# Kernel tuning notes

Hardware: AMD Instinct MI355X
Metric: run time of the kernel (lower is better)

## Reference

```python
import jax, jax.numpy as jnp
import numpy as np

D_MODEL = 2048
N_HEADS = 16
D_K = D_MODEL // N_HEADS
MAX_SEQ_LEN = 2048


def _rotary_tables(dim, max_seq_len):
    angular_freq = (1.0 / 10000.0) ** jnp.linspace(0.0, 1.0, dim // 2, dtype=jnp.float32)
    t = jnp.arange(max_seq_len, dtype=jnp.float32)
    theta = jnp.einsum('i,j->ij', t, angular_freq)  # [S, dk/2]
    return jnp.cos(theta), jnp.sin(theta)


def _apply_rotary(x, cos, sin):
    # x: [B, H, S, dk]; cos/sin: [S, dk/2]
    seq_len = x.shape[-2]
    c = cos[:seq_len][None, None]
    s = sin[:seq_len][None, None]
    x1, x2 = jnp.split(x, 2, axis=-1)
    y1 = x1 * c - x2 * s
    y2 = x1 * s + x2 * c
    return jnp.concatenate([y1, y2], axis=-1).astype(x.dtype)


def setup_inputs() -> dict:
    key = jax.random.key(0)
    k_x, k_qkv, k_o = jax.random.split(key, 3)
    B, S = 2, 2048
    x = jax.random.normal(k_x, (B, S, D_MODEL), dtype=jnp.float32)
    scale = 1.0 / np.sqrt(D_MODEL)
    w_qkv = jax.random.normal(k_qkv, (3 * D_MODEL, D_MODEL), dtype=jnp.float32) * scale
    w_o = jax.random.normal(k_o, (D_MODEL, D_MODEL), dtype=jnp.float32) * scale
    return {"x": x, "w_qkv": w_qkv, "w_o": w_o}


def reference(x, w_qkv, w_o):
    B, S, _ = x.shape
    cos, sin = _rotary_tables(D_K, MAX_SEQ_LEN)
    qkv = jnp.einsum('bsd,ed->bse', x, w_qkv)  # [B, S, 3*d_model]
    qkv = qkv.reshape(B, S, 3, N_HEADS, D_K).transpose(2, 0, 3, 1, 4)  # [3,B,H,S,dk]
    Q, K, V = qkv[0], qkv[1], qkv[2]
    Q = _apply_rotary(Q, cos, sin)
    K = _apply_rotary(K, cos, sin)
    scale = 1.0 / np.sqrt(D_K)
    scores = jnp.einsum('bhqd,bhkd->bhqk', Q, K) * scale
    causal = jnp.tril(jnp.ones((S, S), dtype=bool))
    scores = jnp.where(causal[None, None], scores, jnp.finfo(scores.dtype).min)
    attn = jax.nn.softmax(scores, axis=-1)
    out = jnp.einsum('bhqk,bhkd->bhqd', attn, V)  # [B,H,S,dk]
    out = out.transpose(0, 2, 1, 3).reshape(B, S, D_MODEL)
    return jnp.einsum('bsd,ed->bse', out, w_o)
```

## Files before the change

kernel.cpp:

```cpp
#include <hip/hip_runtime.h>
#include <hip/hip_bf16.h>


typedef __bf16 bf16;
typedef __bf16 bf16x4 __attribute__((ext_vector_type(4)));
typedef __bf16 bf16x8 __attribute__((ext_vector_type(8)));
typedef float f32x4 __attribute__((ext_vector_type(4)));
typedef float f32x16 __attribute__((ext_vector_type(16)));
typedef int i32x4 __attribute__((ext_vector_type(4)));

#define DEV __device__ __forceinline__

DEV void gll16(const void* g, void* lds_base_wave_uniform) {
  __builtin_amdgcn_global_load_lds((const __attribute__((address_space(1))) void*)g,
                                   (__attribute__((address_space(3))) void*)lds_base_wave_uniform,
                                   16, 0, 0);
}

DEV f32x4 mfma16(bf16x8 a, bf16x8 b, f32x4 c) {
  return __builtin_amdgcn_mfma_f32_16x16x32_bf16(a, b, c, 0, 0, 0);
}
DEV f32x16 mfma32(bf16x8 a, bf16x8 b, f32x16 c) {
  return __builtin_amdgcn_mfma_f32_32x32x16_bf16(a, b, c, 0, 0, 0);
}

DEV int cvtpk(float lo, float hi) {
  int r;
  asm("v_cvt_pk_bf16_f32 %0, %1, %2" : "=v"(r) : "v"(lo), "v"(hi));
  return r;
}

__global__ __launch_bounds__(256) void prep_all(const float* __restrict__ x,
                                                const float* __restrict__ wqkv,
                                                const float* __restrict__ wo,
                                                bf16* __restrict__ xb,
                                                bf16* __restrict__ wqkvb,
                                                bf16* __restrict__ wob,
                                                float* __restrict__ ctab,
                                                float* __restrict__ stab) {
  const int b = blockIdx.x;
  if (b < 12288) {
    const float* in;
    bf16* out;
    int bb = b;
    if (b < 4096) {
      in = x; out = xb;
    } else if (b < 10240) {
      in = wqkv; out = wqkvb; bb -= 4096;
    } else {
      in = wo; out = wob; bb -= 10240;
    }
    const int i = (bb * 256 + threadIdx.x) << 3;
    float4 a = *(const float4*)(in + i);
    float4 c = *(const float4*)(in + i + 4);
    bf16x8 o;
    o[0] = (bf16)a.x; o[1] = (bf16)a.y; o[2] = (bf16)a.z; o[3] = (bf16)a.w;
    o[4] = (bf16)c.x; o[5] = (bf16)c.y; o[6] = (bf16)c.z; o[7] = (bf16)c.w;
    *(bf16x8*)(out + i) = o;
  } else {
    const int id = (b - 12288) * 256 + threadIdx.x;
    const int s = id >> 6, j = id & 63;
    float freq = powf(10000.0f, -(float)j / 63.0f);
    float th = (float)s * freq;
    ctab[id] = cosf(th);
    stab[id] = sinf(th);
  }
}

__global__ __launch_bounds__(512, 2) void gemm384(const bf16* __restrict__ A,
                                                  const bf16* __restrict__ Bt,
                                                  bf16* __restrict__ q_out,
                                                  bf16* __restrict__ k_out,
                                                  bf16* __restrict__ v_out,
                                                  const float* __restrict__ ctab,
                                                  const float* __restrict__ stab) {
  constexpr int K = 2048, NKT = 64;
  constexpr int BUFB = 40960;
  __shared__ char lds[3 * BUFB];
  const int id = blockIdx.x;
  const int swz = (id & 7) * 32 + (id >> 3);
  const int bx = swz & 15, by = swz >> 4;
  const int m0 = by << 8;
  const int n0 = bx * 384;
  const int tid = threadIdx.x, w = tid >> 6, l = tid & 63;
  const int wm = w >> 2, wn = w & 3;
  const int lsl = (l & 7) ^ ((l >> 3) & 7);
  const int srow = ((l >> 3) << 1) + (lsl >> 2);
  const int scol = (lsl & 3) << 3;

  auto STAGE = [&](int t, char* base) {
    const int k0 = t << 5;
#pragma unroll
    for (int c = 0; c < 2; ++c) {
      const int row = (c << 7) + (w << 4) + srow;
      gll16(A + (size_t)(m0 + row) * K + k0 + scol, base + (c << 13) + (w << 10));
    }
#pragma unroll
    for (int c = 0; c < 3; ++c) {
      const int row = (c << 7) + (w << 4) + srow;
      gll16(Bt + (size_t)(n0 + row) * K + k0 + scol, base + 16384 + (c << 13) + (w << 10));
    }
  };

  f32x4 acc[8][6] = {};

  STAGE(0, (char*)lds);
  STAGE(1, (char*)lds + BUFB);
  asm volatile("s_waitcnt vmcnt(5)" ::: "memory");
  __builtin_amdgcn_s_barrier();

#pragma unroll 1
  for (int t = 0, bi = 0, bj = 2; t < NKT; ++t) {
    char* rbase = (char*)lds + bi * BUFB;
    bf16x8 bfr[6];
#pragma unroll
    for (int j = 0; j < 6; ++j) {
      const int row = ((j >> 1) << 7) + ((j & 1) << 6) + (wn << 4) + (l & 15);
      const int sr = row >> 1;
      bfr[j] = *(const bf16x8*)(rbase + 16384 + sr * 128 +
                                (((((row & 1) << 2) | (l >> 4)) ^ (sr & 7)) << 4));
    }
    bf16x8 af[4];
#pragma unroll
    for (int i = 0; i < 4; ++i) {
      const int row = (wm << 7) + (i << 4) + (l & 15);
      const int sr = row >> 1;
      af[i] = *(const bf16x8*)(rbase + sr * 128 +
                               (((((row & 1) << 2) | (l >> 4)) ^ (sr & 7)) << 4));
    }
    if (t + 2 < NKT) STAGE(t + 2, (char*)lds + bj * BUFB);
    asm volatile("s_waitcnt lgkmcnt(0)" ::: "memory");
    __builtin_amdgcn_sched_barrier(0);
    __builtin_amdgcn_s_setprio(1);
#pragma unroll
    for (int i = 0; i < 4; ++i)
#pragma unroll
      for (int j = 0; j < 6; ++j)
        acc[i][j] = mfma16(af[i], bfr[j], acc[i][j]);
    __builtin_amdgcn_s_setprio(0);
#pragma unroll
    for (int i = 0; i < 4; ++i) {
      const int row = (wm << 7) + 64 + (i << 4) + (l & 15);
      const int sr = row >> 1;
      af[i] = *(const bf16x8*)(rbase + sr * 128 +
                               (((((row & 1) << 2) | (l >> 4)) ^ (sr & 7)) << 4));
    }
    asm volatile("s_waitcnt lgkmcnt(0)" ::: "memory");
    __builtin_amdgcn_sched_barrier(0);
    __builtin_amdgcn_s_setprio(1);
#pragma unroll
    for (int i = 0; i < 4; ++i)
#pragma unroll
      for (int j = 0; j < 6; ++j)
        acc[4 + i][j] = mfma16(af[i], bfr[j], acc[4 + i][j]);
    __builtin_amdgcn_s_setprio(0);
    if (t + 2 < NKT) {
      asm volatile("s_waitcnt vmcnt(5)" ::: "memory");
    } else if (t + 2 == NKT) {
      asm volatile("s_waitcnt vmcnt(0)" ::: "memory");
    }
    __builtin_amdgcn_sched_barrier(0);
    __builtin_amdgcn_s_barrier();
    bi = (bi == 2) ? 0 : bi + 1;
    bj = (bj == 2) ? 0 : bj + 1;
  }

  const int d2 = (wn << 4) + (l & 15);
#pragma unroll
  for (int i = 0; i < 8; ++i) {
    const int mbase = m0 + (wm << 7) + (i << 4) + ((l >> 4) << 2);
    const int b_ = mbase >> 11, sbase = mbase & 2047;
    float cc[4], ss[4];
    if (((n0 + 256) >> 11) == 1 || (n0 >> 11) == 1) {
#pragma unroll
      for (int r = 0; r < 4; ++r) {
        cc[r] = ctab[((sbase + r) << 6) + d2];
        ss[r] = stab[((sbase + r) << 6) + d2];
      }
    }
#pragma unroll
    for (int p = 0; p < 3; ++p) {
      const int nb = n0 + (p << 7);
      const int which = nb >> 11;
      const int h = (nb >> 7) & 15;
      if (which == 0) {
        const size_t base = (((size_t)((b_ << 4) | h)) * 2048 + sbase) * 128;
#pragma unroll
        for (int r = 0; r < 4; ++r) {
          q_out[base + ((size_t)r << 7) + d2]      = (bf16)acc[i][2 * p][r];
          q_out[base + ((size_t)r << 7) + d2 + 64] = (bf16)acc[i][2 * p + 1][r];
        }
      } else if (which == 1) {
        const size_t base = (((size_t)((b_ << 4) | h)) * 2048 + sbase) * 128;
#pragma unroll
        for (int r = 0; r < 4; ++r) {
          const float x1 = acc[i][2 * p][r], x2 = acc[i][2 * p + 1][r];
          k_out[base + ((size_t)r << 7) + d2]      = (bf16)(x1 * cc[r] - x2 * ss[r]);
          k_out[base + ((size_t)r << 7) + d2 + 64] = (bf16)(x1 * ss[r] + x2 * cc[r]);
        }
      } else {
        bf16x4 v1, v2;
#pragma unroll
        for (int r = 0; r < 4; ++r) {
          v1[r] = (bf16)acc[i][2 * p][r];
          v2[r] = (bf16)acc[i][2 * p + 1][r];
        }
        const size_t hb = ((size_t)((b_ << 4) | h) << 18);
        *(bf16x4*)(v_out + hb + ((size_t)d2 << 11) + sbase) = v1;
        *(bf16x4*)(v_out + hb + ((size_t)(d2 + 64) << 11) + sbase) = v2;
      }
    }
  }
}

template <int NTN>
__global__ __launch_bounds__(256, 2) void gemm_o(const bf16* __restrict__ A,
                                                 const bf16* __restrict__ Bt,
                                                 float* __restrict__ f_out) {
  constexpr int K = 2048, NKT = 64;
  constexpr int BUFB = 16384;
  __shared__ char lds[3 * BUFB];
  const int nwg = 32 * NTN;
  const int id = blockIdx.x;
  const int swz = (id & 7) * (nwg >> 3) + (id >> 3);
  const int bx = swz % NTN, by = swz / NTN;
  const int m0 = by << 7, n0 = bx << 7;
  const int tid = threadIdx.x, w = tid >> 6, l = tid & 63;
  const int wm = w >> 1, wn = w & 1;
  const int lsl = (l & 7) ^ ((l >> 3) & 7);
  const int srow = ((l >> 3) << 1) + (lsl >> 2);
  const int scol = (lsl & 3) << 3;

  auto STAGE = [&](int t, char* base) {
    const int k0 = t << 5;
#pragma unroll
    for (int c = 0; c < 2; ++c) {
      const int row = (c << 6) + (w << 4) + srow;
      gll16(A + (size_t)(m0 + row) * K + k0 + scol, base + (c << 12) + (w << 10));
      gll16(Bt + (size_t)(n0 + row) * K + k0 + scol, base + 8192 + (c << 12) + (w << 10));
    }
  };

  f32x4 acc[4][4] = {};

  STAGE(0, (char*)lds);
  STAGE(1, (char*)lds + BUFB);
  asm volatile("s_waitcnt vmcnt(4)" ::: "memory");
  __builtin_amdgcn_s_barrier();

#pragma unroll 1
  for (int t = 0, bi = 0, bj = 2; t < NKT; ++t) {
    char* rbase = (char*)lds + bi * BUFB;
    bf16x8 af[4], bfr[4];
#pragma unroll
    for (int i = 0; i < 4; ++i) {
      const int row = (wm << 6) + (i << 4) + (l & 15);
      const int sr = row >> 1;
      af[i] = *(const bf16x8*)(rbase + sr * 128 +
                               (((((row & 1) << 2) | (l >> 4)) ^ (sr & 7)) << 4));
    }
#pragma unroll
    for (int j = 0; j < 4; ++j) {
      const int row = (wn << 6) + (j << 4) + (l & 15);
      const int sr = row >> 1;
      bfr[j] = *(const bf16x8*)(rbase + 8192 + sr * 128 +
                                (((((row & 1) << 2) | (l >> 4)) ^ (sr & 7)) << 4));
    }
    if (t + 2 < NKT) STAGE(t + 2, (char*)lds + bj * BUFB);
    asm volatile("s_waitcnt lgkmcnt(0)" ::: "memory");
    __builtin_amdgcn_sched_barrier(0);
    __builtin_amdgcn_s_setprio(1);
#pragma unroll
    for (int i = 0; i < 4; ++i)
#pragma unroll
      for (int j = 0; j < 4; ++j)
        acc[i][j] = mfma16(af[i], bfr[j], acc[i][j]);
    __builtin_amdgcn_s_setprio(0);
    if (t + 2 < NKT) {
      asm volatile("s_waitcnt vmcnt(4)" ::: "memory");
    } else if (t + 2 == NKT) {
      asm volatile("s_waitcnt vmcnt(0)" ::: "memory");
    }
    __builtin_amdgcn_sched_barrier(0);
    __builtin_amdgcn_s_barrier();
    bi = (bi == 2) ? 0 : bi + 1;
    bj = (bj == 2) ? 0 : bj + 1;
  }

#pragma unroll
  for (int i = 0; i < 4; ++i)
#pragma unroll
    for (int j = 0; j < 4; ++j)
#pragma unroll
      for (int r = 0; r < 4; ++r) {
        const int m = m0 + (wm << 6) + (i << 4) + ((l >> 4) << 2) + r;
        const int n = n0 + (wn << 6) + (j << 4) + (l & 15);
        f_out[(size_t)m * 2048 + n] = acc[i][j][r];
      }
}

__global__ __launch_bounds__(256, 2) void attn_kernel(const bf16* __restrict__ Qb,
                                                      const bf16* __restrict__ Kb,
                                                      const bf16* __restrict__ Vt,
                                                      bf16* __restrict__ Ao,
                                                      const float* __restrict__ ctab,
                                                      const float* __restrict__ stab) {
  constexpr int S = 2048;
  __shared__ bf16 Ks[2][64 * 128];
  __shared__ bf16 Vs[2][128 * 64];
  const int id = blockIdx.x;
  const int swz = (id & 7) * 32 + (id >> 3);
  const int bh = swz >> 3;
  const int pp = swz & 7;
  const int ntA = (pp + 1) << 1;
  const int NT = 34;
  const int tid = threadIdx.x, w = tid >> 6, l = tid & 63;
  const int hi = l >> 5;
  const bf16* Qp = Qb + ((size_t)bh << 18);
  const bf16* Kp = Kb + ((size_t)bh << 18);
  const bf16* Vp = Vt + ((size_t)bh << 18);

  auto STAGE_KV = [&](int kv0, int bufi) {
    char* Kbase = (char*)Ks + (bufi << 14);
    char* Vbase = (char*)Vs + (bufi << 14);
#pragma unroll
    for (int i = 0; i < 4; ++i) {
      const int rk = (w << 4) + (i << 2) + (l >> 4);
      gll16(Kp + ((size_t)(kv0 + rk) << 7) + (((l & 15) ^ (rk & 7)) << 3),
            Kbase + (w << 12) + (i << 10));
      const int rv = (w << 5) + (i << 3) + (l >> 3);
      gll16(Vp + (size_t)rv * S + kv0 + (((l & 7) ^ (rv & 7)) << 3),
            Vbase + (w << 12) + (i << 10));
    }
  };

  bf16x8 qf[8];
  auto LOAD_Q = [&](int q0_) {
    const int sq = q0_ + (w << 5) + (l & 31);
#pragma unroll
    for (int kt = 0; kt < 8; ++kt)
      qf[kt] = *(const bf16x8*)(Qp + ((size_t)sq << 7) + (kt << 4) + (hi << 3));
    const float QS = 0.08838834764831845f * 1.4426950408889634f;
#pragma unroll
    for (int kt = 0; kt < 4; ++kt) {
      const int d2 = (kt << 4) + (hi << 3);
      const float* cp = ctab + (sq << 6) + d2;
      const float* sp = stab + (sq << 6) + d2;
      float4 c0 = *(const float4*)cp, c1 = *(const float4*)(cp + 4);
      float4 s0 = *(const float4*)sp, s1 = *(const float4*)(sp + 4);
      const float cA[8] = {c0.x, c0.y, c0.z, c0.w, c1.x, c1.y, c1.z, c1.w};
      const float sA[8] = {s0.x, s0.y, s0.z, s0.w, s1.x, s1.y, s1.z, s1.w};
      const bf16x8 lo = qf[kt], up = qf[kt + 4];
#pragma unroll
      for (int j2 = 0; j2 < 8; ++j2) {
        const float a = (float)lo[j2], b2 = (float)up[j2];
        qf[kt][j2]     = (bf16)((a * cA[j2] - b2 * sA[j2]) * QS);
        qf[kt + 4][j2] = (bf16)((a * sA[j2] + b2 * cA[j2]) * QS);
      }
    }
  };

  f32x16 o[4] = {};
  float mrun = -3e38f, lrun = 0.f;
  int q0 = pp << 7;

  auto EPILOGUE = [&](int q0_) {
    const float rinv = 1.0f / lrun;
    const int b = bh >> 4, h = bh & 15;
    const int sq = q0_ + (w << 5) + (l & 31);
    bf16* Arow = Ao + (((size_t)(b * S + sq)) << 11) + (h << 7);
#pragma unroll
    for (int dt = 0; dt < 4; ++dt)
#pragma unroll
      for (int g = 0; g < 4; ++g) {
        bf16x4 ov;
#pragma unroll
        for (int r = 0; r < 4; ++r) ov[r] = (bf16)(o[dt][(g << 2) + r] * rinv);
        *(bf16x4*)(Arow + (dt << 5) + (g << 3) + (hi << 2)) = ov;
      }
  };

  STAGE_KV(0, 0);
  LOAD_Q(q0);
  __syncthreads();

  int bufi = 0;
#pragma unroll 1
  for (int ti = 0; ti < NT; ++ti, bufi ^= 1) {
    const int kv0 = ((ti < ntA) ? ti : ti - ntA) << 6;
    if (ti + 1 < NT) {
      const int kv0n = ((ti + 1 < ntA) ? ti + 1 : ti + 1 - ntA) << 6;
      STAGE_KV(kv0n, bufi ^ 1);
    }
    const int qminw = q0 + (w << 5);
    if (kv0 <= qminw + 31) {
      const char* Kbase = (const char*)Ks + (bufi << 14);
      const char* Vbase = (const char*)Vs + (bufi << 14);
      f32x16 sc0 = {}, sc1 = {};
      __builtin_amdgcn_s_setprio(1);
#pragma unroll
      for (int kt = 0; kt < 8; ++kt) {
        const int rk0 = l & 31;
        const int coff = ((kt << 5) + (hi << 4));
        bf16x8 k0 = *(const bf16x8*)(Kbase + (rk0 << 8) + (coff ^ ((rk0 & 7) << 4)));
        bf16x8 k1 = *(const bf16x8*)(Kbase + ((rk0 + 32) << 8) + (coff ^ ((rk0 & 7) << 4)));
        sc0 = mfma32(k0, qf[kt], sc0);
        sc1 = mfma32(k1, qf[kt], sc1);
      }
      __builtin_amdgcn_s_setprio(0);
      if (kv0 + 63 > qminw) {
        const int qg = qminw + (l & 31);
#pragma unroll
        for (int r = 0; r < 16; ++r) {
          const int kvr = kv0 + (r & 3) + ((r >> 2) << 3) + (hi << 2);
          if (kvr > qg) sc0[r] = -3e38f;
          if (kvr + 32 > qg) sc1[r] = -3e38f;
        }
      }
      f32x16 mm;
#pragma unroll
      for (int r = 0; r < 16; ++r) mm[r] = fmaxf(sc0[r], sc1[r]);
#pragma unroll
      for (int off = 8; off; off >>= 1)
#pragma unroll
        for (int r = 0; r < off; ++r) mm[r] = fmaxf(mm[r], mm[r + off]);
      float mx = mm[0];
      mx = fmaxf(mx, __shfl_xor(mx, 32));
      const float mnew = fmaxf(mrun, mx);
      if (!__all(mx <= mrun)) {
        const float alpha = exp2f(mrun - mnew);
        lrun *= alpha;
#pragma unroll
        for (int dt = 0; dt < 4; ++dt) o[dt] *= alpha;
      }
      mrun = mnew;
      float p0 = 0.f, p1 = 0.f, p2 = 0.f, p3 = 0.f;
#pragma unroll
      for (int r = 0; r < 16; r += 2) {
        sc0[r] = exp2f(sc0[r] - mnew); sc0[r + 1] = exp2f(sc0[r + 1] - mnew);
        sc1[r] = exp2f(sc1[r] - mnew); sc1[r + 1] = exp2f(sc1[r + 1] - mnew);
        p0 += sc0[r]; p1 += sc0[r + 1]; p2 += sc1[r]; p3 += sc1[r + 1];
      }
      float ps = (p0 + p1) + (p2 + p3);
      ps += __shfl_xor(ps, 32);
      lrun += ps;
#pragma unroll
      for (int ks = 0; ks < 4; ++ks) {
        const f32x16& s = (ks & 2) ? sc1 : sc0;
        const int rb = (ks & 1) << 3;
        int pa_ = cvtpk(s[rb + 0], s[rb + 1]);
        int pb_ = cvtpk(s[rb + 2], s[rb + 3]);
        int pc_ = cvtpk(s[rb + 4], s[rb + 5]);
        int pd_ = cvtpk(s[rb + 6], s[rb + 7]);
        int sa = __shfl_xor(pa_, 32), sb = __shfl_xor(pb_, 32);
        int sc_ = __shfl_xor(pc_, 32), sd = __shfl_xor(pd_, 32);
        i32x4 pi;
        pi[0] = hi ? sc_ : pa_;
        pi[1] = hi ? sd : pb_;
        pi[2] = hi ? pc_ : sa;
        pi[3] = hi ? pd_ : sb;
        const bf16x8 pf = __builtin_bit_cast(bf16x8, pi);
        __builtin_amdgcn_s_setprio(1);
#pragma unroll
        for (int dt = 0; dt < 4; ++dt) {
          const int rd = (dt << 5) + (l & 31);
          const bf16x8 vf = *(const bf16x8*)(Vbase + (rd << 7) +
                                             (((ks << 5) + (hi << 4)) ^ ((rd & 7) << 4)));
          o[dt] = mfma32(vf, pf, o[dt]);
        }
        __builtin_amdgcn_s_setprio(0);
      }
    }
    if (ti == ntA - 1) {
      EPILOGUE(q0);
      q0 = (15 - pp) << 7;
#pragma unroll
      for (int dt = 0; dt < 4; ++dt)
#pragma unroll
        for (int r = 0; r < 16; ++r) o[dt][r] = 0.f;
      mrun = -3e38f; lrun = 0.f;
      LOAD_Q(q0);
    }
    __syncthreads();
  }
  EPILOGUE(q0);
}

extern "C" void kernel_launch(void* const* d_in, const int* in_sizes, int n_in,
                              void* d_out, int out_size, void* d_ws, size_t ws_size,
                              hipStream_t stream) {
  const float* x = (const float*)d_in[0];
  const float* w_qkv = (const float*)d_in[1];
  const float* w_o = (const float*)d_in[2];
  float* out = (float*)d_out;
  char* ws = (char*)d_ws;

  bf16* xb    = (bf16*)(ws);
  bf16* wqkvb = (bf16*)(ws + (16ull << 20));
  bf16* wob   = (bf16*)(ws + (40ull << 20));
  bf16* Qb    = (bf16*)(ws + (48ull << 20));
  bf16* Kb    = (bf16*)(ws + (64ull << 20));
  bf16* Vt    = (bf16*)(ws + (80ull << 20));
  bf16* Ao    = (bf16*)(ws + (96ull << 20));
  float* ctab = (float*)(ws + (112ull << 20));
  float* stab = (float*)(ws + (113ull << 20));

  prep_all<<<12800, 256, 0, stream>>>(x, w_qkv, w_o, xb, wqkvb, wob, ctab, stab);
  gemm384<<<256, 512, 0, stream>>>(xb, wqkvb, Qb, Kb, Vt, ctab, stab);
  attn_kernel<<<256, 256, 0, stream>>>(Qb, Kb, Vt, Ao, ctab, stab);
  gemm_o<16><<<512, 256, 0, stream>>>(Ao, wob, out);
}
```

Measured before the change: 244.1 us.

## Triple-buffer K/V tiles in attention with two-ahead prefetch and partial vmcnt waits

Grows the K/V shared-memory staging from two buffers to three and prefetches the tile two iterations ahead. The full __syncthreads is replaced by a partial s_waitcnt vmcnt(8) plus s_barrier, so only the older tile's loads must land before the next iteration. This hides more global-load latency behind the MFMA work. LDS use rises from 64KB to 96KB per block, which may limit the two-blocks-per-CU occupancy, and the hand-tuned vmcnt counts depend on the exact number of outstanding loads, including the Q reload in the middle of the loop.

```diff
diff --git a/kernel.cpp b/kernel.cpp
--- a/kernel.cpp
+++ b/kernel.cpp
@@ -306,8 +306,8 @@
                                                       const float* __restrict__ ctab,
                                                       const float* __restrict__ stab) {
   constexpr int S = 2048;
-  __shared__ bf16 Ks[2][64 * 128];
-  __shared__ bf16 Vs[2][128 * 64];
+  __shared__ bf16 Ks[3][64 * 128];
+  __shared__ bf16 Vs[3][128 * 64];
   const int id = blockIdx.x;
   const int swz = (id & 7) * 32 + (id >> 3);
   const int bh = swz >> 3;
@@ -320,9 +320,11 @@
   const bf16* Kp = Kb + ((size_t)bh << 18);
   const bf16* Vp = Vt + ((size_t)bh << 18);
 
+  auto KVSEQ = [&](int ti) { return ((ti < ntA) ? ti : ti - ntA) << 6; };
+
   auto STAGE_KV = [&](int kv0, int bufi) {
-    char* Kbase = (char*)Ks + (bufi << 14);
-    char* Vbase = (char*)Vs + (bufi << 14);
+    char* Kbase = (char*)Ks + bufi * 16384;
+    char* Vbase = (char*)Vs + bufi * 16384;
 #pragma unroll
     for (int i = 0; i < 4; ++i) {
       const int rk = (w << 4) + (i << 2) + (l >> 4);
@@ -380,22 +382,25 @@
       }
   };
 
-  STAGE_KV(0, 0);
   LOAD_Q(q0);
-  __syncthreads();
-
-  int bufi = 0;
+  STAGE_KV(KVSEQ(0), 0);
+  STAGE_KV(KVSEQ(1), 1);
+  asm volatile("s_waitcnt vmcnt(8)" ::: "memory");
+  __builtin_amdgcn_sched_barrier(0);
+  __builtin_amdgcn_s_barrier();
+
+  int rb = 0;
 #pragma unroll 1
-  for (int ti = 0; ti < NT; ++ti, bufi ^= 1) {
-    const int kv0 = ((ti < ntA) ? ti : ti - ntA) << 6;
-    if (ti + 1 < NT) {
-      const int kv0n = ((ti + 1 < ntA) ? ti + 1 : ti + 1 - ntA) << 6;
-      STAGE_KV(kv0n, bufi ^ 1);
-    }
+  for (int ti = 0; ti < NT; ++ti) {
+    if (ti + 2 < NT) {
+      const int sb = (rb == 0) ? 2 : rb - 1;
+      STAGE_KV(KVSEQ(ti + 2), sb);
+    }
+    const int kv0 = KVSEQ(ti);
     const int qminw = q0 + (w << 5);
     if (kv0 <= qminw + 31) {
-      const char* Kbase = (const char*)Ks + (bufi << 14);
-      const char* Vbase = (const char*)Vs + (bufi << 14);
+      const char* Kbase = (const char*)Ks + rb * 16384;
+      const char* Vbase = (const char*)Vs + rb * 16384;
       f32x16 sc0 = {}, sc1 = {};
       __builtin_amdgcn_s_setprio(1);
 #pragma unroll
@@ -447,18 +452,18 @@
 #pragma unroll
       for (int ks = 0; ks < 4; ++ks) {
         const f32x16& s = (ks & 2) ? sc1 : sc0;
-        const int rb = (ks & 1) << 3;
-        int pa_ = cvtpk(s[rb + 0], s[rb + 1]);
-        int pb_ = cvtpk(s[rb + 2], s[rb + 3]);
-        int pc_ = cvtpk(s[rb + 4], s[rb + 5]);
-        int pd_ = cvtpk(s[rb + 6], s[rb + 7]);
-        int sa = __shfl_xor(pa_, 32), sb = __shfl_xor(pb_, 32);
+        const int rbp = (ks & 1) << 3;
+        int pa_ = cvtpk(s[rbp + 0], s[rbp + 1]);
+        int pb_ = cvtpk(s[rbp + 2], s[rbp + 3]);
+        int pc_ = cvtpk(s[rbp + 4], s[rbp + 5]);
+        int pd_ = cvtpk(s[rbp + 6], s[rbp + 7]);
+        int sa = __shfl_xor(pa_, 32), sb2 = __shfl_xor(pb_, 32);
         int sc_ = __shfl_xor(pc_, 32), sd = __shfl_xor(pd_, 32);
         i32x4 pi;
         pi[0] = hi ? sc_ : pa_;
         pi[1] = hi ? sd : pb_;
         pi[2] = hi ? pc_ : sa;
-        pi[3] = hi ? pd_ : sb;
+        pi[3] = hi ? pd_ : sb2;
         const bf16x8 pf = __builtin_bit_cast(bf16x8, pi);
         __builtin_amdgcn_s_setprio(1);
 #pragma unroll
@@ -481,7 +486,14 @@
       mrun = -3e38f; lrun = 0.f;
       LOAD_Q(q0);
     }
-    __syncthreads();
+    if (ti + 2 < NT) {
+      asm volatile("s_waitcnt vmcnt(8)" ::: "memory");
+    } else if (ti + 2 == NT) {
+      asm volatile("s_waitcnt vmcnt(0)" ::: "memory");
+    }
+    __builtin_amdgcn_sched_barrier(0);
+    __builtin_amdgcn_s_barrier();
+    rb = (rb == 2) ? 0 : rb + 1;
   }
   EPILOGUE(q0);
 }
```

New measurement: 259.6 us. 1.06x slower.
